# Performance work log

Hardware: AMD Instinct MI355X
Metric: run time of the kernel (lower is better)

Reference implementation:

```python
import jax, jax.numpy as jnp
import numpy as np

B, N, D, NUM_K = 128, 1024, 64, 8


def setup_inputs() -> dict:
    key = jax.random.key(0)
    k1, k2, k3 = jax.random.split(key, 3)
    nodes = jax.random.normal(k1, (B, N, D), dtype=jnp.float32)
    # xavier_uniform over (in_dims, in_dims) fan: bound = sqrt(6 / (N + N))
    bound = float(np.sqrt(6.0 / (N + N)))
    weight = jax.random.uniform(k2, (NUM_K, N, N), dtype=jnp.float32,
                                minval=-bound, maxval=bound)
    graph_shift = jax.random.normal(k3, (N, N), dtype=jnp.float32) / np.sqrt(N)
    return {"nodes": nodes, "weight": weight, "graph_shift": graph_shift}


def reference(nodes, weight, graph_shift):
    """Polynomial graph filter: out[b] = sum_k W_k @ S^k @ X_b.

    Since sum_k W_k S^k X = (sum_k W_k S^k) X, we fuse all taps into one
    N x N operator A, then apply a single batched GEMM over the batch.
    """
    n = nodes.shape[1]
    eye = jnp.eye(n, dtype=nodes.dtype)

    def step(S, Wk):
        # emit W_k @ S^k, carry S^{k+1}
        return S @ graph_shift, Wk @ S

    _, Mk = jax.lax.scan(step, eye, weight)   # [num_k, N, N]
    A = Mk.sum(axis=0)                        # fused filter operator [N, N]
    return jnp.einsum('nm,bmd->bnd', A, nodes)  # [B, N, D]
```

## Files before the change

### kernel.cpp

```cpp
#include <hip/hip_runtime.h>
#include <stdint.h>


#define NN 1024
#define NBATCH 128
#define DDIM 64

typedef float floatx4 __attribute__((ext_vector_type(4)));
typedef _Float16 f16x8 __attribute__((ext_vector_type(8)));
typedef unsigned short u16;

__device__ __forceinline__ u16 f2h(float f) {
  union { _Float16 h; u16 u; } v; v.h = (_Float16)f; return v.u;
}
__device__ __forceinline__ float h2f(u16 u) {
  union { _Float16 h; u16 u; } v; v.u = u; return (float)v.h;
}

__device__ __forceinline__ void gll16(const void* g, void* l) {
  __builtin_amdgcn_global_load_lds(
      (const __attribute__((address_space(1))) void*)g,
      (__attribute__((address_space(3))) void*)l, 16, 0, 0);
}

template <int ROWS>
__device__ __forceinline__ void stage64(const u16* __restrict__ g, u16* lds,
                                        int wave, int lane) {
  const int r = lane >> 3, c = lane & 7;
  const int sw = (c ^ r) * 8;
#pragma unroll
  for (int i = 0; i < ROWS / 32; ++i) {
    const int rb = wave * (ROWS / 4) + i * 8;
    gll16(g + (size_t)(rb + r) * NN + sw, lds + rb * 64);
  }
}

struct CvtJob { const float* src; u16* rm; u16* cm; };
struct CvtJobs { CvtJob j[5]; };

__global__ __launch_bounds__(256) void cvt_kernel(CvtJobs jobs) {
  CvtJob jb = jobs.j[blockIdx.z];
  int idx4 = blockIdx.x * 256 + threadIdx.x;
  int e = idx4 * 4;
  int row = e >> 10, col = e & (NN - 1);
  float4 f = ((const float4*)jb.src)[idx4];
  u16 h[4] = { f2h(f.x), f2h(f.y), f2h(f.z), f2h(f.w) };
  uint2 p;
  p.x = (uint32_t)h[0] | ((uint32_t)h[1] << 16);
  p.y = (uint32_t)h[2] | ((uint32_t)h[3] << 16);
  *(uint2*)&jb.rm[e] = p;
  if (jb.cm) {
#pragma unroll
    for (int i = 0; i < 4; ++i) jb.cm[(size_t)(col + i) * NN + row] = h[i];
  }
}

__global__ __launch_bounds__(256) void transpose_x(const float* __restrict__ X,
                                                   u16* __restrict__ XT) {
  __shared__ u16 T[64][72];
  const int k0 = blockIdx.x * 64;
  const int b = blockIdx.y;
  const int t = threadIdx.x;
#pragma unroll
  for (int it = 0; it < 4; ++it) {
    int kr = (t >> 4) + it * 16;
    int d4 = (t & 15) * 4;
    float4 f = *(const float4*)&X[((size_t)b * NN + k0 + kr) * DDIM + d4];
    T[d4 + 0][kr] = f2h(f.x);
    T[d4 + 1][kr] = f2h(f.y);
    T[d4 + 2][kr] = f2h(f.z);
    T[d4 + 3][kr] = f2h(f.w);
  }
  __syncthreads();
#pragma unroll
  for (int it = 0; it < 2; ++it) {
    int d = (t >> 3) + it * 32;
    int kc = (t & 7) * 8;
    *(uint4*)&XT[((size_t)b * DDIM + d) * NN + k0 + kc] = *(uint4*)&T[d][kc];
  }
}

struct GemmJob {
  const u16* A;
  const u16* B;
  const float* addF;
  const u16* addH;
  u16* outRm;
  u16* outCm;
  float* outP;
};
struct GemmJobs { GemmJob j[5]; };

template <int BM, int BN, int WM, int WN, int KSPLIT>
__global__ __launch_bounds__(256) void gemm_f16(GemmJobs jobs) {
  const GemmJob jb = jobs.j[blockIdx.z / KSPLIT];
  const int chunk = blockIdx.z % KSPLIT;
  __shared__ u16 As[2][BM * 64], Bs[2][BN * 64];
  const int t = threadIdx.x, wave = t >> 6, lane = t & 63;
  const int wm = wave / WN, wn = wave % WN;
  const int lm = lane & 15, q = lane >> 4;
  const int bm = blockIdx.x * BM, bn = blockIdx.y * BN;
  constexpr int MI = BM / (WM * 16), NI = BN / (WN * 16);
  constexpr int KTPB = 16 / KSPLIT;
  floatx4 acc[MI][NI] = {};

  const u16* Ag = jb.A + (size_t)bm * NN + chunk * KTPB * 64;
  const u16* Bg = jb.B + (size_t)bn * NN + chunk * KTPB * 64;

  if constexpr (KSPLIT == 1) {
    if (jb.addF) {
#pragma unroll
      for (int mi = 0; mi < MI; ++mi)
#pragma unroll
        for (int ni = 0; ni < NI; ++ni)
#pragma unroll
          for (int r = 0; r < 4; ++r) {
            int row = bm + wm * (BM / WM) + mi * 16 + q * 4 + r;
            int col = bn + wn * (BN / WN) + ni * 16 + lm;
            acc[mi][ni][r] = jb.addF[(size_t)row * NN + col];
          }
    } else if (jb.addH) {
#pragma unroll
      for (int mi = 0; mi < MI; ++mi)
#pragma unroll
        for (int ni = 0; ni < NI; ++ni)
#pragma unroll
          for (int r = 0; r < 4; ++r) {
            int row = bm + wm * (BM / WM) + mi * 16 + q * 4 + r;
            int col = bn + wn * (BN / WN) + ni * 16 + lm;
            acc[mi][ni][r] = h2f(jb.addH[(size_t)row * NN + col]);
          }
    }
  }

  stage64<BM>(Ag, As[0], wave, lane);
  stage64<BN>(Bg, Bs[0], wave, lane);
  __syncthreads();

  for (int kk = 0; kk < KTPB; ++kk) {
    const int cur = kk & 1;
    if (kk + 1 < KTPB) {
      stage64<BM>(Ag + (kk + 1) * 64, As[cur ^ 1], wave, lane);
      stage64<BN>(Bg + (kk + 1) * 64, Bs[cur ^ 1], wave, lane);
    }
#pragma unroll
    for (int ks = 0; ks < 2; ++ks) {
      const int st = ((ks * 4 + q) ^ (lm & 7)) * 8;
      f16x8 bf[NI];
#pragma unroll
      for (int ni = 0; ni < NI; ++ni)
        bf[ni] = *(const f16x8*)&Bs[cur][(wn * (BN / WN) + ni * 16 + lm) * 64 + st];
#pragma unroll
      for (int mi = 0; mi < MI; ++mi) {
        f16x8 a = *(const f16x8*)&As[cur][(wm * (BM / WM) + mi * 16 + lm) * 64 + st];
#pragma unroll
        for (int ni = 0; ni < NI; ++ni)
          acc[mi][ni] = __builtin_amdgcn_mfma_f32_16x16x32_f16(a, bf[ni], acc[mi][ni], 0, 0, 0);
      }
    }
    __syncthreads();
  }

  if constexpr (KSPLIT > 1) {
    float* p = jb.outP + (size_t)chunk * NN * NN;
#pragma unroll
    for (int mi = 0; mi < MI; ++mi)
#pragma unroll
      for (int ni = 0; ni < NI; ++ni)
#pragma unroll
        for (int r = 0; r < 4; ++r) {
          int row = bm + wm * (BM / WM) + mi * 16 + q * 4 + r;
          int col = bn + wn * (BN / WN) + ni * 16 + lm;
          p[(size_t)row * NN + col] = acc[mi][ni][r];
        }
  } else {
#pragma unroll
    for (int mi = 0; mi < MI; ++mi)
#pragma unroll
      for (int ni = 0; ni < NI; ++ni)
#pragma unroll
        for (int r = 0; r < 4; ++r) {
          int row = bm + wm * (BM / WM) + mi * 16 + q * 4 + r;
          int col = bn + wn * (BN / WN) + ni * 16 + lm;
          size_t rm = (size_t)row * NN + col;
          u16 h = f2h(acc[mi][ni][r]);
          if (jb.outRm) jb.outRm[rm] = h;
          if (jb.outCm) jb.outCm[(size_t)col * NN + row] = h;
        }
  }
}

__global__ __launch_bounds__(256) void combine_A(const float* __restrict__ parts,
                                                 const u16* __restrict__ v0,
                                                 u16* __restrict__ A) {
  int e = (blockIdx.x * 256 + threadIdx.x) * 4;
  float4 s = *(const float4*)&parts[e];
#pragma unroll
  for (int z = 1; z < 4; ++z) {
    float4 p = *(const float4*)&parts[(size_t)z * NN * NN + e];
    s.x += p.x; s.y += p.y; s.z += p.z; s.w += p.w;
  }
  uint2 h = *(const uint2*)&v0[e];
  uint2 o;
  o.x = (uint32_t)f2h(s.x + h2f((u16)h.x)) |
        ((uint32_t)f2h(s.y + h2f((u16)(h.x >> 16))) << 16);
  o.y = (uint32_t)f2h(s.z + h2f((u16)h.y)) |
        ((uint32_t)f2h(s.w + h2f((u16)(h.y >> 16))) << 16);
  *(uint2*)&A[e] = o;
}

__global__ __launch_bounds__(256) void apply_gemm(const u16* __restrict__ A,
                                                  const u16* __restrict__ XT,
                                                  float* __restrict__ out) {
  __shared__ u16 As[2][128 * 64], Xs[2][128 * 64];
  const int t = threadIdx.x, wave = t >> 6, lane = t & 63;
  const int wm = wave >> 1, wn = wave & 1;
  const int lm = lane & 15, q = lane >> 4;
  const int bn = blockIdx.x * 128;
  const int bm = blockIdx.y * 128;
  floatx4 acc[4][4] = {};
  const u16* Ag = A + (size_t)bm * NN;
  const u16* Xg = XT + (size_t)bn * NN;

  stage64<128>(Ag, As[0], wave, lane);
  stage64<128>(Xg, Xs[0], wave, lane);
  __syncthreads();

  for (int kt = 0; kt < 16; ++kt) {
    const int cur = kt & 1;
    if (kt + 1 < 16) {
      stage64<128>(Ag + (kt + 1) * 64, As[cur ^ 1], wave, lane);
      stage64<128>(Xg + (kt + 1) * 64, Xs[cur ^ 1], wave, lane);
    }
#pragma unroll
    for (int ks = 0; ks < 2; ++ks) {
      const int st = ((ks * 4 + q) ^ (lm & 7)) * 8;
      f16x8 xf[4];
#pragma unroll
      for (int ni = 0; ni < 4; ++ni)
        xf[ni] = *(const f16x8*)&Xs[cur][(wn * 64 + ni * 16 + lm) * 64 + st];
#pragma unroll
      for (int mi = 0; mi < 4; ++mi) {
        f16x8 a = *(const f16x8*)&As[cur][(wm * 64 + mi * 16 + lm) * 64 + st];
#pragma unroll
        for (int ni = 0; ni < 4; ++ni)
          acc[mi][ni] = __builtin_amdgcn_mfma_f32_16x16x32_f16(a, xf[ni], acc[mi][ni], 0, 0, 0);
      }
    }
    __syncthreads();
  }

#pragma unroll
  for (int mi = 0; mi < 4; ++mi)
#pragma unroll
    for (int ni = 0; ni < 4; ++ni)
#pragma unroll
      for (int r = 0; r < 4; ++r) {
        int row = bm + wm * 64 + mi * 16 + q * 4 + r;
        int col = bn + wn * 64 + ni * 16 + lm;
        out[((size_t)(col >> 6) * NN + row) * DDIM + (col & 63)] =
            acc[mi][ni][r];
      }
}

extern "C" void kernel_launch(void* const* d_in, const int* in_sizes, int n_in,
                              void* d_out, int out_size, void* d_ws, size_t ws_size,
                              hipStream_t stream) {
  const float* nodes  = (const float*)d_in[0];
  const float* weight = (const float*)d_in[1];
  const float* gs     = (const float*)d_in[2];
  float* out = (float*)d_out;
  u16* ws = (u16*)d_ws;
  const size_t MB = (size_t)NN * NN;
  auto buf = [&](int i) -> u16* { return ws + (size_t)i * MB; };

  CvtJobs cv{};
  cv.j[0] = { gs,              buf(0), buf(1) };
  cv.j[1] = { weight + 1 * MB, buf(2), nullptr };
  cv.j[2] = { weight + 3 * MB, buf(3), nullptr };
  cv.j[3] = { weight + 5 * MB, buf(4), nullptr };
  cv.j[4] = { weight + 7 * MB, buf(5), nullptr };
  cvt_kernel<<<dim3(NN * NN / 1024, 1, 5), 256, 0, stream>>>(cv);

  GemmJobs g1{};
  g1.j[0] = { buf(0), buf(1), nullptr,         nullptr, buf(6),  buf(7),  nullptr };
  g1.j[1] = { buf(2), buf(1), weight + 0 * MB, nullptr, buf(8),  nullptr, nullptr };
  g1.j[2] = { buf(3), buf(1), weight + 2 * MB, nullptr, buf(9),  nullptr, nullptr };
  g1.j[3] = { buf(4), buf(1), weight + 4 * MB, nullptr, buf(10), nullptr, nullptr };
  g1.j[4] = { buf(5), buf(1), weight + 6 * MB, nullptr, buf(11), nullptr, nullptr };
  gemm_f16<64, 128, 2, 2, 1><<<dim3(16, 8, 5), 256, 0, stream>>>(g1);

  u16* XT = buf(16);
  transpose_x<<<dim3(16, NBATCH), 256, 0, stream>>>(nodes, XT);

  GemmJobs g2{};
  g2.j[0] = { buf(6),  buf(7), nullptr, nullptr, nullptr, buf(12), nullptr };
  g2.j[1] = { buf(9),  buf(7), nullptr, buf(8),  buf(13), nullptr, nullptr };
  g2.j[2] = { buf(11), buf(7), nullptr, buf(10), buf(14), nullptr, nullptr };
  gemm_f16<64, 64, 2, 2, 1><<<dim3(16, 16, 3), 256, 0, stream>>>(g2);

  float* parts = (float*)buf(24);
  GemmJobs g3{};
  g3.j[0] = { buf(14), buf(12), nullptr, nullptr, nullptr, nullptr, parts };
  gemm_f16<64, 64, 2, 2, 4><<<dim3(16, 16, 4), 256, 0, stream>>>(g3);

  combine_A<<<dim3(NN * NN / 1024), 256, 0, stream>>>(parts, buf(13), buf(15));

  apply_gemm<<<dim3(64, 8), 256, 0, stream>>>(buf(15), XT, out);
}
```

Measured before the change: 192.9 us.

## Merge prep kernels and drop split-K partial buffer for final tap GEMM

Combines the fp16 conversion and the X transpose into a single prep kernel launch. It also removes split-K from the third GEMM, so that GEMM adds the fp16 addend in its prologue and writes A directly, which eliminates the fp32 partial buffers and the combine kernel. This cuts two launches and a large fp32 round trip through memory. The cost is that the last GEMM runs with four times fewer blocks, each doing the full K loop.

```diff
diff --git a/kernel.cpp b/kernel.cpp
--- a/kernel.cpp
+++ b/kernel.cpp
@@ -38,45 +38,48 @@
 struct CvtJob { const float* src; u16* rm; u16* cm; };
 struct CvtJobs { CvtJob j[5]; };
 
-__global__ __launch_bounds__(256) void cvt_kernel(CvtJobs jobs) {
-  CvtJob jb = jobs.j[blockIdx.z];
-  int idx4 = blockIdx.x * 256 + threadIdx.x;
-  int e = idx4 * 4;
-  int row = e >> 10, col = e & (NN - 1);
-  float4 f = ((const float4*)jb.src)[idx4];
-  u16 h[4] = { f2h(f.x), f2h(f.y), f2h(f.z), f2h(f.w) };
-  uint2 p;
-  p.x = (uint32_t)h[0] | ((uint32_t)h[1] << 16);
-  p.y = (uint32_t)h[2] | ((uint32_t)h[3] << 16);
-  *(uint2*)&jb.rm[e] = p;
-  if (jb.cm) {
-#pragma unroll
-    for (int i = 0; i < 4; ++i) jb.cm[(size_t)(col + i) * NN + row] = h[i];
-  }
-}
-
-__global__ __launch_bounds__(256) void transpose_x(const float* __restrict__ X,
+__global__ __launch_bounds__(256) void prep_kernel(CvtJobs jobs,
+                                                   const float* __restrict__ X,
                                                    u16* __restrict__ XT) {
   __shared__ u16 T[64][72];
-  const int k0 = blockIdx.x * 64;
-  const int b = blockIdx.y;
+  const int bid = blockIdx.x;
   const int t = threadIdx.x;
-#pragma unroll
-  for (int it = 0; it < 4; ++it) {
-    int kr = (t >> 4) + it * 16;
-    int d4 = (t & 15) * 4;
-    float4 f = *(const float4*)&X[((size_t)b * NN + k0 + kr) * DDIM + d4];
-    T[d4 + 0][kr] = f2h(f.x);
-    T[d4 + 1][kr] = f2h(f.y);
-    T[d4 + 2][kr] = f2h(f.z);
-    T[d4 + 3][kr] = f2h(f.w);
-  }
-  __syncthreads();
-#pragma unroll
-  for (int it = 0; it < 2; ++it) {
-    int d = (t >> 3) + it * 32;
-    int kc = (t & 7) * 8;
-    *(uint4*)&XT[((size_t)b * DDIM + d) * NN + k0 + kc] = *(uint4*)&T[d][kc];
+  if (bid < 5120) {
+    CvtJob jb = jobs.j[bid >> 10];
+    int idx4 = (bid & 1023) * 256 + t;
+    int e = idx4 * 4;
+    int row = e >> 10, col = e & (NN - 1);
+    float4 f = ((const float4*)jb.src)[idx4];
+    u16 h[4] = { f2h(f.x), f2h(f.y), f2h(f.z), f2h(f.w) };
+    uint2 p;
+    p.x = (uint32_t)h[0] | ((uint32_t)h[1] << 16);
+    p.y = (uint32_t)h[2] | ((uint32_t)h[3] << 16);
+    *(uint2*)&jb.rm[e] = p;
+    if (jb.cm) {
+#pragma unroll
+      for (int i = 0; i < 4; ++i) jb.cm[(size_t)(col + i) * NN + row] = h[i];
+    }
+  } else {
+    const int tb = bid - 5120;
+    const int k0 = (tb & 15) * 64;
+    const int b = tb >> 4;
+#pragma unroll
+    for (int it = 0; it < 4; ++it) {
+      int kr = (t >> 4) + it * 16;
+      int d4 = (t & 15) * 4;
+      float4 f = *(const float4*)&X[((size_t)b * NN + k0 + kr) * DDIM + d4];
+      T[d4 + 0][kr] = f2h(f.x);
+      T[d4 + 1][kr] = f2h(f.y);
+      T[d4 + 2][kr] = f2h(f.z);
+      T[d4 + 3][kr] = f2h(f.w);
+    }
+    __syncthreads();
+#pragma unroll
+    for (int it = 0; it < 2; ++it) {
+      int d = (t >> 3) + it * 32;
+      int kc = (t & 7) * 8;
+      *(uint4*)&XT[((size_t)b * DDIM + d) * NN + k0 + kc] = *(uint4*)&T[d][kc];
+    }
   }
 }
 
@@ -87,59 +90,54 @@
   const u16* addH;
   u16* outRm;
   u16* outCm;
-  float* outP;
 };
 struct GemmJobs { GemmJob j[5]; };
 
-template <int BM, int BN, int WM, int WN, int KSPLIT>
+template <int BM, int BN, int WM, int WN>
 __global__ __launch_bounds__(256) void gemm_f16(GemmJobs jobs) {
-  const GemmJob jb = jobs.j[blockIdx.z / KSPLIT];
-  const int chunk = blockIdx.z % KSPLIT;
+  const GemmJob jb = jobs.j[blockIdx.z];
   __shared__ u16 As[2][BM * 64], Bs[2][BN * 64];
   const int t = threadIdx.x, wave = t >> 6, lane = t & 63;
   const int wm = wave / WN, wn = wave % WN;
   const int lm = lane & 15, q = lane >> 4;
   const int bm = blockIdx.x * BM, bn = blockIdx.y * BN;
   constexpr int MI = BM / (WM * 16), NI = BN / (WN * 16);
-  constexpr int KTPB = 16 / KSPLIT;
   floatx4 acc[MI][NI] = {};
 
-  const u16* Ag = jb.A + (size_t)bm * NN + chunk * KTPB * 64;
-  const u16* Bg = jb.B + (size_t)bn * NN + chunk * KTPB * 64;
-
-  if constexpr (KSPLIT == 1) {
-    if (jb.addF) {
-#pragma unroll
-      for (int mi = 0; mi < MI; ++mi)
-#pragma unroll
-        for (int ni = 0; ni < NI; ++ni)
-#pragma unroll
-          for (int r = 0; r < 4; ++r) {
-            int row = bm + wm * (BM / WM) + mi * 16 + q * 4 + r;
-            int col = bn + wn * (BN / WN) + ni * 16 + lm;
-            acc[mi][ni][r] = jb.addF[(size_t)row * NN + col];
-          }
-    } else if (jb.addH) {
-#pragma unroll
-      for (int mi = 0; mi < MI; ++mi)
-#pragma unroll
-        for (int ni = 0; ni < NI; ++ni)
-#pragma unroll
-          for (int r = 0; r < 4; ++r) {
-            int row = bm + wm * (BM / WM) + mi * 16 + q * 4 + r;
-            int col = bn + wn * (BN / WN) + ni * 16 + lm;
-            acc[mi][ni][r] = h2f(jb.addH[(size_t)row * NN + col]);
-          }
-    }
+  const u16* Ag = jb.A + (size_t)bm * NN;
+  const u16* Bg = jb.B + (size_t)bn * NN;
+
+  if (jb.addF) {
+#pragma unroll
+    for (int mi = 0; mi < MI; ++mi)
+#pragma unroll
+      for (int ni = 0; ni < NI; ++ni)
+#pragma unroll
+        for (int r = 0; r < 4; ++r) {
+          int row = bm + wm * (BM / WM) + mi * 16 + q * 4 + r;
+          int col = bn + wn * (BN / WN) + ni * 16 + lm;
+          acc[mi][ni][r] = jb.addF[(size_t)row * NN + col];
+        }
+  } else if (jb.addH) {
+#pragma unroll
+    for (int mi = 0; mi < MI; ++mi)
+#pragma unroll
+      for (int ni = 0; ni < NI; ++ni)
+#pragma unroll
+        for (int r = 0; r < 4; ++r) {
+          int row = bm + wm * (BM / WM) + mi * 16 + q * 4 + r;
+          int col = bn + wn * (BN / WN) + ni * 16 + lm;
+          acc[mi][ni][r] = h2f(jb.addH[(size_t)row * NN + col]);
+        }
   }
 
   stage64<BM>(Ag, As[0], wave, lane);
   stage64<BN>(Bg, Bs[0], wave, lane);
   __syncthreads();
 
-  for (int kk = 0; kk < KTPB; ++kk) {
+  for (int kk = 0; kk < 16; ++kk) {
     const int cur = kk & 1;
-    if (kk + 1 < KTPB) {
+    if (kk + 1 < 16) {
       stage64<BM>(Ag + (kk + 1) * 64, As[cur ^ 1], wave, lane);
       stage64<BN>(Bg + (kk + 1) * 64, Bs[cur ^ 1], wave, lane);
     }
@@ -161,52 +159,19 @@
     __syncthreads();
   }
 
-  if constexpr (KSPLIT > 1) {
-    float* p = jb.outP + (size_t)chunk * NN * NN;
-#pragma unroll
-    for (int mi = 0; mi < MI; ++mi)
-#pragma unroll
-      for (int ni = 0; ni < NI; ++ni)
-#pragma unroll
-        for (int r = 0; r < 4; ++r) {
-          int row = bm + wm * (BM / WM) + mi * 16 + q * 4 + r;
-          int col = bn + wn * (BN / WN) + ni * 16 + lm;
-          p[(size_t)row * NN + col] = acc[mi][ni][r];
-        }
-  } else {
-#pragma unroll
-    for (int mi = 0; mi < MI; ++mi)
-#pragma unroll
-      for (int ni = 0; ni < NI; ++ni)
-#pragma unroll
-        for (int r = 0; r < 4; ++r) {
-          int row = bm + wm * (BM / WM) + mi * 16 + q * 4 + r;
-          int col = bn + wn * (BN / WN) + ni * 16 + lm;
-          size_t rm = (size_t)row * NN + col;
-          u16 h = f2h(acc[mi][ni][r]);
-          if (jb.outRm) jb.outRm[rm] = h;
-          if (jb.outCm) jb.outCm[(size_t)col * NN + row] = h;
-        }
-  }
-}
-
-__global__ __launch_bounds__(256) void combine_A(const float* __restrict__ parts,
-                                                 const u16* __restrict__ v0,
-                                                 u16* __restrict__ A) {
-  int e = (blockIdx.x * 256 + threadIdx.x) * 4;
-  float4 s = *(const float4*)&parts[e];
-#pragma unroll
-  for (int z = 1; z < 4; ++z) {
-    float4 p = *(const float4*)&parts[(size_t)z * NN * NN + e];
-    s.x += p.x; s.y += p.y; s.z += p.z; s.w += p.w;
-  }
-  uint2 h = *(const uint2*)&v0[e];
-  uint2 o;
-  o.x = (uint32_t)f2h(s.x + h2f((u16)h.x)) |
-        ((uint32_t)f2h(s.y + h2f((u16)(h.x >> 16))) << 16);
-  o.y = (uint32_t)f2h(s.z + h2f((u16)h.y)) |
-        ((uint32_t)f2h(s.w + h2f((u16)(h.y >> 16))) << 16);
-  *(uint2*)&A[e] = o;
+#pragma unroll
+  for (int mi = 0; mi < MI; ++mi)
+#pragma unroll
+    for (int ni = 0; ni < NI; ++ni)
+#pragma unroll
+      for (int r = 0; r < 4; ++r) {
+        int row = bm + wm * (BM / WM) + mi * 16 + q * 4 + r;
+        int col = bn + wn * (BN / WN) + ni * 16 + lm;
+        size_t rm = (size_t)row * NN + col;
+        u16 h = f2h(acc[mi][ni][r]);
+        if (jb.outRm) jb.outRm[rm] = h;
+        if (jb.outCm) jb.outCm[(size_t)col * NN + row] = h;
+      }
 }
 
 __global__ __launch_bounds__(256) void apply_gemm(const u16* __restrict__ A,
@@ -274,37 +239,32 @@
   const size_t MB = (size_t)NN * NN;
   auto buf = [&](int i) -> u16* { return ws + (size_t)i * MB; };
 
+  u16* XT = buf(16);
   CvtJobs cv{};
   cv.j[0] = { gs,              buf(0), buf(1) };
   cv.j[1] = { weight + 1 * MB, buf(2), nullptr };
   cv.j[2] = { weight + 3 * MB, buf(3), nullptr };
   cv.j[3] = { weight + 5 * MB, buf(4), nullptr };
   cv.j[4] = { weight + 7 * MB, buf(5), nullptr };
-  cvt_kernel<<<dim3(NN * NN / 1024, 1, 5), 256, 0, stream>>>(cv);
+  prep_kernel<<<dim3(5120 + 2048), 256, 0, stream>>>(cv, nodes, XT);
 
   GemmJobs g1{};
-  g1.j[0] = { buf(0), buf(1), nullptr,         nullptr, buf(6),  buf(7),  nullptr };
-  g1.j[1] = { buf(2), buf(1), weight + 0 * MB, nullptr, buf(8),  nullptr, nullptr };
-  g1.j[2] = { buf(3), buf(1), weight + 2 * MB, nullptr, buf(9),  nullptr, nullptr };
-  g1.j[3] = { buf(4), buf(1), weight + 4 * MB, nullptr, buf(10), nullptr, nullptr };
-  g1.j[4] = { buf(5), buf(1), weight + 6 * MB, nullptr, buf(11), nullptr, nullptr };
-  gemm_f16<64, 128, 2, 2, 1><<<dim3(16, 8, 5), 256, 0, stream>>>(g1);
-
-  u16* XT = buf(16);
-  transpose_x<<<dim3(16, NBATCH), 256, 0, stream>>>(nodes, XT);
+  g1.j[0] = { buf(0), buf(1), nullptr,         nullptr, buf(6),  buf(7)  };
+  g1.j[1] = { buf(2), buf(1), weight + 0 * MB, nullptr, buf(8),  nullptr };
+  g1.j[2] = { buf(3), buf(1), weight + 2 * MB, nullptr, buf(9),  nullptr };
+  g1.j[3] = { buf(4), buf(1), weight + 4 * MB, nullptr, buf(10), nullptr };
+  g1.j[4] = { buf(5), buf(1), weight + 6 * MB, nullptr, buf(11), nullptr };
+  gemm_f16<64, 128, 2, 2><<<dim3(16, 8, 5), 256, 0, stream>>>(g1);
 
   GemmJobs g2{};
-  g2.j[0] = { buf(6),  buf(7), nullptr, nullptr, nullptr, buf(12), nullptr };
-  g2.j[1] = { buf(9),  buf(7), nullptr, buf(8),  buf(13), nullptr, nullptr };
-  g2.j[2] = { buf(11), buf(7), nullptr, buf(10), buf(14), nullptr, nullptr };
-  gemm_f16<64, 64, 2, 2, 1><<<dim3(16, 16, 3), 256, 0, stream>>>(g2);
-
-  float* parts = (float*)buf(24);
+  g2.j[0] = { buf(6),  buf(7), nullptr, nullptr, nullptr, buf(12) };
+  g2.j[1] = { buf(9),  buf(7), nullptr, buf(8),  buf(13), nullptr };
+  g2.j[2] = { buf(11), buf(7), nullptr, buf(10), buf(14), nullptr };
+  gemm_f16<64, 64, 2, 2><<<dim3(16, 16, 3), 256, 0, stream>>>(g2);
+
   GemmJobs g3{};
-  g3.j[0] = { buf(14), buf(12), nullptr, nullptr, nullptr, nullptr, parts };
-  gemm_f16<64, 64, 2, 2, 4><<<dim3(16, 16, 4), 256, 0, stream>>>(g3);
-
-  combine_A<<<dim3(NN * NN / 1024), 256, 0, stream>>>(parts, buf(13), buf(15));
+  g3.j[0] = { buf(14), buf(12), nullptr, buf(13), buf(15), nullptr };
+  gemm_f16<64, 64, 2, 2><<<dim3(16, 16, 1), 256, 0, stream>>>(g3);
 
   apply_gemm<<<dim3(64, 8), 256, 0, stream>>>(buf(15), XT, out);
 }
```

Result: no change. 193.6 us (+0.4%).
